# Optimization experiments

Measured on AMD Instinct MI355X. Metric: run time of the kernel, lower is better.

The kernel has to match this reference:

```python
import jax, jax.numpy as jnp
import numpy as np

D, L, DIM, G = 64, 64, 512, 256      # dialogues, utterances/dialogue, feat dim, graph dim
TOPK_FRAC = 0.2
TAU = 0.07


def setup_inputs() -> dict:
    key = jax.random.key(0)
    ks = jax.random.split(key, 7)
    N = D * L
    t = jax.random.normal(ks[0], (N, DIM), dtype=jnp.float32)
    a = jax.random.normal(ks[1], (N, DIM), dtype=jnp.float32)
    v = jax.random.normal(ks[2], (N, DIM), dtype=jnp.float32)
    W_fc = jax.random.normal(ks[3], (DIM, G), dtype=jnp.float32) / np.sqrt(DIM)
    b_fc = jnp.zeros((G,), dtype=jnp.float32)
    W_h = jax.random.normal(ks[4], (G, G), dtype=jnp.float32) / np.sqrt(G)
    b_h = jnp.zeros((G,), dtype=jnp.float32)
    dia_len = np.full((D,), L, dtype=np.int64)  # uniform dialogue lengths
    return {"t": t, "a": a, "v": v, "W_fc": W_fc, "b_fc": b_fc,
            "W_h": W_h, "b_h": b_h, "dia_len": dia_len}


def _contrastive_loss(x, y, tau=TAU):
    # symmetric InfoNCE with matched-index positives
    xn = x / (jnp.linalg.norm(x, axis=-1, keepdims=True) + 1e-8)
    yn = y / (jnp.linalg.norm(y, axis=-1, keepdims=True) + 1e-8)
    sim = (xn @ yn.T) / tau                     # [N, N]
    pos_xy = jnp.diagonal(jax.nn.log_softmax(sim, axis=1))
    pos_yx = jnp.diagonal(jax.nn.log_softmax(sim, axis=0))
    return -(pos_xy.mean() + pos_yx.mean()) / 2.0


def _forward(t, a, v, W_fc, b_fc, W_h, b_h, dia_len):
    dl = np.asarray(dia_len)
    d, l = dl.shape[0], int(dl[0])              # uniform lengths assumed
    m = 3 * l                                   # nodes (and hyperedges) per dialogue
    k = int(l * TOPK_FRAC)
    dim = t.shape[-1]

    # per-dialogue node features in original order [t_i; a_i; v_i]
    feat = jnp.concatenate([t.reshape(d, l, dim),
                            a.reshape(d, l, dim),
                            v.reshape(d, l, dim)], axis=1)   # [d, m, dim]

    # squared euclidean distances (same ordering as torch.cdist for top-k smallest)
    sq = jnp.sum(feat * feat, axis=-1)                        # [d, m]
    d2 = sq[:, :, None] + sq[:, None, :] - 2.0 * jnp.einsum('dmf,dnf->dmn', feat, feat)
    d2 = jax.lax.stop_gradient(jnp.maximum(d2, 0.0))
    _, idx = jax.lax.top_k(-d2, k)                            # [d, m, k] nearest nodes

    # boolean incidence H[d, e, n] = node n participates in hyperedge e
    # (set-union dedup in the original == boolean OR here)
    node_ids = jnp.arange(m)
    H_nb = (idx[..., None] == node_ids).any(axis=2)           # [d, m, m]
    u = node_ids // 3                                         # central utterance of edge j
    cent = ((node_ids[None, :] == u[:, None]) |
            (node_ids[None, :] == u[:, None] + l) |
            (node_ids[None, :] == u[:, None] + 2 * l))        # [m, m]
    H = (H_nb | cent[None]).astype(feat.dtype)                # [d, m, m]

    # fc projection
    X = feat @ W_fc + b_fc                                    # [d, m, G]

    # hypergraph conv: node -> hyperedge (mean) -> node (mean), then Linear+ReLU
    deg_e = H.sum(axis=2, keepdims=True)                      # [d, m, 1]
    E = jnp.einsum('den,dng->deg', H, X) / deg_e              # edge features
    deg_v = H.sum(axis=1)[..., None]                          # [d, m, 1]
    Y = jnp.einsum('den,deg->dng', H, E) / deg_v              # node features
    out = jax.nn.relu(Y @ W_h + b_h)                          # [d, m, G]

    # reverse_features: regroup by modality across dialogues
    tn = out[:, :l].reshape(d * l, -1)
    an = out[:, l:2 * l].reshape(d * l, -1)
    vn = out[:, 2 * l:].reshape(d * l, -1)
    out_cat = jnp.concatenate([tn, an, vn], axis=1)           # [N, 3G]

    loss = (_contrastive_loss(tn, an) + _contrastive_loss(tn, vn)
            + _contrastive_loss(an, vn)) / 3.0
    return out_cat, loss


def reference(t, a, v, W_fc, b_fc, W_h, b_h, dia_len):
    return _forward(t, a, v, W_fc, b_fc, W_h, b_h, dia_len)
```

## Files before the change

### kernel.cpp

```cpp
#include <hip/hip_runtime.h>
#include <math.h>

#define NDIAL 64
#define M3    192
#define DIMF  512
#define GDIM  256
#define NROW  4096
#define TOPK  12
#define INV_TAU (1.0f/0.07f)

typedef __attribute__((ext_vector_type(8))) short bf16x8;
typedef __attribute__((ext_vector_type(4))) float f32x4;
typedef _Float16 f16x8 __attribute__((ext_vector_type(8)));
typedef _Float16 f16x4v __attribute__((ext_vector_type(4)));
typedef __attribute__((address_space(3))) ushort lds_us;
typedef const __attribute__((address_space(1))) ushort gm_us;

__device__ __forceinline__ ushort f2bf(float f) {
    unsigned u = __float_as_uint(f);
    unsigned r = (u + 0x7fff + ((u >> 16) & 1)) >> 16;
    return (ushort)r;
}

template<int KDIM>
__device__ __forceinline__ void mm64bt(
    const float* __restrict__ A, int lda,
    const float* __restrict__ B, int ldb,
    float acc[4][4])
{
    __shared__ float As[64][33];
    __shared__ float Bs[32][68];
    const int tid = threadIdx.x;
    const int tx = tid & 15, ty = tid >> 4;

#pragma unroll
    for (int r = 0; r < 4; r++)
#pragma unroll
        for (int c = 0; c < 4; c++) acc[r][c] = 0.f;

    for (int k0 = 0; k0 < KDIM; k0 += 32) {
#pragma unroll
        for (int i = 0; i < 2; i++) {
            int f = tid + i * 256;
            int m = f >> 3, k4 = f & 7;
            const float4 v4 = *(const float4*)(A + (size_t)m * lda + k0 + k4 * 4);
            As[m][k4 * 4 + 0] = v4.x;
            As[m][k4 * 4 + 1] = v4.y;
            As[m][k4 * 4 + 2] = v4.z;
            As[m][k4 * 4 + 3] = v4.w;
        }
#pragma unroll
        for (int i = 0; i < 2; i++) {
            int f = tid + i * 256;
            int n = f >> 3, k4 = f & 7;
            const float4 v4 = *(const float4*)(B + (size_t)n * ldb + k0 + k4 * 4);
            Bs[k4 * 4 + 0][n] = v4.x;
            Bs[k4 * 4 + 1][n] = v4.y;
            Bs[k4 * 4 + 2][n] = v4.z;
            Bs[k4 * 4 + 3][n] = v4.w;
        }
        __syncthreads();
#pragma unroll
        for (int kk = 0; kk < 32; kk++) {
            float4 b = *(const float4*)&Bs[kk][tx * 4];
#pragma unroll
            for (int r = 0; r < 4; r++) {
                float av = As[ty * 4 + r][kk];
                acc[r][0] += av * b.x;
                acc[r][1] += av * b.y;
                acc[r][2] += av * b.z;
                acc[r][3] += av * b.w;
            }
        }
        __syncthreads();
    }
}

template<int KD, int NW>
__device__ __forceinline__ void hgemm_bt(const _Float16* __restrict__ A, int lda,
                                         const _Float16* __restrict__ B, int ldb,
                                         f32x4 acc[4][4]) {
    __shared__ __align__(16) _Float16 As[64 * 40];
    __shared__ __align__(16) _Float16 Bs[NW * 64 * 40];
    const int tid = threadIdx.x;
    const int lane = tid & 63, w = tid >> 6;
    const int qd = lane >> 4, l15 = lane & 15;

#pragma unroll
    for (int fm = 0; fm < 4; fm++)
#pragma unroll
        for (int fn = 0; fn < 4; fn++)
            acc[fm][fn] = (f32x4){0.f, 0.f, 0.f, 0.f};

    for (int k0 = 0; k0 < KD; k0 += 32) {
        for (int f = tid; f < 256; f += NW * 64) {
            int row = f >> 2, c8 = f & 3;
            *(float4*)&As[row * 40 + c8 * 8] =
                *(const float4*)&A[(size_t)row * lda + k0 + c8 * 8];
        }
#pragma unroll
        for (int i = 0; i < 4; i++) {
            int f = tid + i * NW * 64;
            int row = f >> 2, c8 = f & 3;
            *(float4*)&Bs[row * 40 + c8 * 8] =
                *(const float4*)&B[(size_t)row * ldb + k0 + c8 * 8];
        }
        __syncthreads();
        f16x8 af[4], bfr[4];
#pragma unroll
        for (int fm = 0; fm < 4; fm++)
            af[fm] = *(const f16x8*)&As[(fm * 16 + l15) * 40 + qd * 8];
#pragma unroll
        for (int fn = 0; fn < 4; fn++)
            bfr[fn] = *(const f16x8*)&Bs[(w * 64 + fn * 16 + l15) * 40 + qd * 8];
#pragma unroll
        for (int fm = 0; fm < 4; fm++)
#pragma unroll
            for (int fn = 0; fn < 4; fn++)
                acc[fm][fn] = __builtin_amdgcn_mfma_f32_16x16x32_f16(
                    af[fm], bfr[fn], acc[fm][fn], 0, 0, 0);
        __syncthreads();
    }
}

__device__ __forceinline__ const float* node_ptr(const float* t, const float* a,
                                                 const float* v, int d, int j) {
    int mod = j >> 6, i = j & 63;
    const float* base = (mod == 0) ? t : (mod == 1) ? a : v;
    return base + (size_t)(d * 64 + i) * DIMF;
}

__global__ void kprep(const float* __restrict__ t, const float* __restrict__ a,
                      const float* __restrict__ v, const float* __restrict__ Wfc,
                      const float* __restrict__ Wh, _Float16* __restrict__ featb,
                      _Float16* __restrict__ WfcT, _Float16* __restrict__ WhT,
                      float* __restrict__ sq, float* __restrict__ rs,
                      float* __restrict__ cs, float* __restrict__ degV,
                      _Float16* __restrict__ HbT) {
    int b = blockIdx.x, tid = threadIdx.x;
    if (b < 6144) {
        int e = (b * 256 + tid) * 4;
        int d = e / (M3 * DIMF);
        int rem = e % (M3 * DIMF);
        int n = rem / DIMF, kk = rem % DIMF;
        int mod = n >> 6, i = n & 63;
        const float* src = ((mod == 0) ? t : (mod == 1) ? a : v)
                           + (size_t)(d * 64 + i) * DIMF + kk;
        float4 x = *(const float4*)src;
        f16x4v o = {(_Float16)x.x, (_Float16)x.y, (_Float16)x.z, (_Float16)x.w};
        *(f16x4v*)&featb[e] = o;
    } else if (b < 6272) {
        int e = ((b - 6144) * 256 + tid) * 4;
        int g = e >> 9, kk = e & 511;
        f16x4v o = {(_Float16)Wfc[(size_t)(kk + 0) * GDIM + g],
                    (_Float16)Wfc[(size_t)(kk + 1) * GDIM + g],
                    (_Float16)Wfc[(size_t)(kk + 2) * GDIM + g],
                    (_Float16)Wfc[(size_t)(kk + 3) * GDIM + g]};
        *(f16x4v*)&WfcT[(size_t)g * DIMF + kk] = o;
    } else if (b < 6336) {
        int e = ((b - 6272) * 256 + tid) * 4;
        int go = e >> 8, g = e & 255;
        f16x4v o = {(_Float16)Wh[(size_t)(g + 0) * GDIM + go],
                    (_Float16)Wh[(size_t)(g + 1) * GDIM + go],
                    (_Float16)Wh[(size_t)(g + 2) * GDIM + go],
                    (_Float16)Wh[(size_t)(g + 3) * GDIM + go]};
        *(f16x4v*)&WhT[(size_t)go * GDIM + g] = o;
    } else if (b < 9408) {
        int lane = tid & 63, wv = tid >> 6;
        int n = (b - 6336) * 4 + wv;
        int d = n / M3, j = n % M3;
        const float4* s4 = (const float4*)node_ptr(t, a, v, d, j);
        float s = 0.f;
#pragma unroll
        for (int q = 0; q < 2; q++) {
            float4 x = s4[lane + q * 64];
            s += x.x * x.x + x.y * x.y + x.z * x.z + x.w * x.w;
        }
        for (int o = 32; o; o >>= 1) s += __shfl_down(s, o);
        if (lane == 0) sq[n] = s;
    } else if (b < 9456) {
        int i = (b - 9408) * 256 + tid;
        rs[i] = 0.f; cs[i] = 0.f; degV[i] = 0.f;
    } else {
        int i = (b - 9456) * 256 + tid;
        ulonglong2 z = {0ull, 0ull};
        *(ulonglong2*)&HbT[(size_t)i * 8] = z;
    }
}

__global__ void k1_d2(const float* __restrict__ t, const float* __restrict__ a,
                      const float* __restrict__ v, const float* __restrict__ sq,
                      float* __restrict__ d2) {
    int tileid = blockIdx.x;
    int d = blockIdx.y;
    int bi = (tileid < 3) ? 0 : (tileid < 5) ? 1 : 2;
    int bj = (tileid < 3) ? tileid : (tileid < 5) ? tileid - 2 : 2;
    const float* A = ((bi == 0) ? t : (bi == 1) ? a : v) + (size_t)d * 64 * DIMF;
    const float* B = ((bj == 0) ? t : (bj == 1) ? a : v) + (size_t)d * 64 * DIMF;
    float acc[4][4];
    mm64bt<DIMF>(A, DIMF, B, DIMF, acc);
    int tx = threadIdx.x & 15, ty = threadIdx.x >> 4;
    const float* sqd = sq + d * M3;
    float* outp = d2 + (size_t)d * M3 * M3;
#pragma unroll
    for (int r = 0; r < 4; r++)
#pragma unroll
        for (int c = 0; c < 4; c++) {
            int il = bi * 64 + ty * 4 + r;
            int jl = bj * 64 + tx * 4 + c;
            float vv = fmaxf(sqd[il] + sqd[jl] - 2.f * acc[r][c], 0.f);
            outp[(size_t)il * M3 + jl] = vv;
            if (bi != bj) outp[(size_t)jl * M3 + il] = vv;
        }
}

__global__ void k2_topk(const float* __restrict__ d2, _Float16* __restrict__ Hb,
                        _Float16* __restrict__ HbT, float* __restrict__ degE,
                        float* __restrict__ degV) {
    int lane = threadIdx.x & 63, wv = threadIdx.x >> 6;
    int r = blockIdx.x * 4 + wv;
    int d = r / M3, e = r % M3;
    const float* row = d2 + (size_t)r * M3;
    float w0 = row[lane], w1 = row[lane + 64], w2 = row[lane + 128];
    bool s0 = false, s1 = false, s2 = false;
#pragma unroll
    for (int it = 0; it < TOPK; it++) {
        float bv = w0; int bi = lane;
        if (w1 < bv) { bv = w1; bi = lane + 64; }
        if (w2 < bv) { bv = w2; bi = lane + 128; }
#pragma unroll
        for (int o = 1; o < 64; o <<= 1) {
            float ov = __shfl_xor(bv, o);
            int   oi = __shfl_xor(bi, o);
            if (ov < bv || (ov == bv && oi < bi)) { bv = ov; bi = oi; }
        }
        if (bi == lane)            { s0 = true; w0 = 3.4e38f; }
        else if (bi == lane + 64)  { s1 = true; w1 = 3.4e38f; }
        else if (bi == lane + 128) { s2 = true; w2 = 3.4e38f; }
    }
    int u = e / 3;
    if (lane == u) { s0 = true; s1 = true; s2 = true; }
    float f0 = s0 ? 1.f : 0.f, f1 = s1 ? 1.f : 0.f, f2 = s2 ? 1.f : 0.f;
    _Float16* Hrow = Hb + (size_t)r * M3;
    Hrow[lane] = (_Float16)f0;
    Hrow[lane + 64] = (_Float16)f1;
    Hrow[lane + 128] = (_Float16)f2;
    float cnt = f0 + f1 + f2;
#pragma unroll
    for (int o = 1; o < 64; o <<= 1) cnt += __shfl_xor(cnt, o);
    if (lane == 0) degE[r] = cnt;
    float* dv = degV + d * M3;
    _Float16* HT = HbT + (size_t)d * M3 * M3;
    if (s0) { atomicAdd(&dv[lane], 1.f);       HT[(size_t)lane * M3 + e] = (_Float16)1.f; }
    if (s1) { atomicAdd(&dv[lane + 64], 1.f);  HT[(size_t)(lane + 64) * M3 + e] = (_Float16)1.f; }
    if (s2) { atomicAdd(&dv[lane + 128], 1.f); HT[(size_t)(lane + 128) * M3 + e] = (_Float16)1.f; }
}

__global__ void k3_x(const _Float16* __restrict__ WfcT, const _Float16* __restrict__ featb,
                     const float* __restrict__ bfc, _Float16* __restrict__ XT) {
    int gb = blockIdx.x, d = blockIdx.y;
    const _Float16* A = WfcT + (size_t)gb * 64 * DIMF;
    const _Float16* B = featb + (size_t)d * M3 * DIMF;
    f32x4 acc[4][4];
    hgemm_bt<DIMF, 3>(A, DIMF, B, DIMF, acc);
    int lane = threadIdx.x & 63, w = threadIdx.x >> 6;
    int qd = lane >> 4, l15 = lane & 15;
    _Float16* out = XT + (size_t)d * GDIM * M3;
#pragma unroll
    for (int fm = 0; fm < 4; fm++)
#pragma unroll
        for (int rg = 0; rg < 4; rg++) {
            int g = gb * 64 + fm * 16 + qd * 4 + rg;
            float bias = bfc[g];
#pragma unroll
            for (int fn = 0; fn < 4; fn++) {
                int n = w * 64 + fn * 16 + l15;
                out[(size_t)g * M3 + n] = (_Float16)(acc[fm][fn][rg] + bias);
            }
        }
}

__global__ void k4_E(const _Float16* __restrict__ XT, const _Float16* __restrict__ Hb,
                     const float* __restrict__ degE, _Float16* __restrict__ ET) {
    int gb = blockIdx.x, d = blockIdx.y;
    const _Float16* A = XT + (size_t)d * GDIM * M3 + (size_t)gb * 64 * M3;
    const _Float16* B = Hb + (size_t)d * M3 * M3;
    f32x4 acc[4][4];
    hgemm_bt<M3, 3>(A, M3, B, M3, acc);
    int lane = threadIdx.x & 63, w = threadIdx.x >> 6;
    int qd = lane >> 4, l15 = lane & 15;
    float ide[4];
#pragma unroll
    for (int fn = 0; fn < 4; fn++)
        ide[fn] = 1.f / degE[d * M3 + w * 64 + fn * 16 + l15];
    _Float16* out = ET + (size_t)d * GDIM * M3;
#pragma unroll
    for (int fm = 0; fm < 4; fm++)
#pragma unroll
        for (int rg = 0; rg < 4; rg++) {
            int g = gb * 64 + fm * 16 + qd * 4 + rg;
#pragma unroll
            for (int fn = 0; fn < 4; fn++) {
                int e = w * 64 + fn * 16 + l15;
                out[(size_t)g * M3 + e] = (_Float16)(acc[fm][fn][rg] * ide[fn]);
            }
        }
}

__global__ void k5_Y(const _Float16* __restrict__ HbT, const _Float16* __restrict__ ET,
                     const float* __restrict__ degV, _Float16* __restrict__ Y) {
    int nb = blockIdx.x, d = blockIdx.y;
    const _Float16* A = HbT + (size_t)d * M3 * M3 + (size_t)nb * 64 * M3;
    const _Float16* B = ET + (size_t)d * GDIM * M3;
    f32x4 acc[4][4];
    hgemm_bt<M3, 4>(A, M3, B, M3, acc);
    int lane = threadIdx.x & 63, w = threadIdx.x >> 6;
    int qd = lane >> 4, l15 = lane & 15;
    _Float16* out = Y + ((size_t)d * M3 + nb * 64) * GDIM;
#pragma unroll
    for (int fm = 0; fm < 4; fm++)
#pragma unroll
        for (int rg = 0; rg < 4; rg++) {
            int ml = fm * 16 + qd * 4 + rg;
            float idv = 1.f / degV[d * M3 + nb * 64 + ml];
#pragma unroll
            for (int fn = 0; fn < 4; fn++) {
                int g = w * 64 + fn * 16 + l15;
                out[(size_t)ml * GDIM + g] = (_Float16)(acc[fm][fn][rg] * idv);
            }
        }
}

__global__ void k6_out(const _Float16* __restrict__ Y, const _Float16* __restrict__ WhT,
                       const float* __restrict__ bh, float* __restrict__ outp) {
    int b = blockIdx.x;
    const _Float16* A = Y + (size_t)b * 64 * GDIM;
    f32x4 acc[4][4];
    hgemm_bt<GDIM, 4>(A, GDIM, WhT, GDIM, acc);
    int lane = threadIdx.x & 63, w = threadIdx.x >> 6;
    int qd = lane >> 4, l15 = lane & 15;
    float bb[4];
#pragma unroll
    for (int fn = 0; fn < 4; fn++)
        bb[fn] = bh[w * 64 + fn * 16 + l15];
#pragma unroll
    for (int fm = 0; fm < 4; fm++)
#pragma unroll
        for (int rg = 0; rg < 4; rg++) {
            int r = b * 64 + fm * 16 + qd * 4 + rg;
            int d = r / M3, n = r % M3;
            int mod = n >> 6, i = n & 63;
            float* orow = outp + (size_t)(d * 64 + i) * 768 + mod * GDIM;
#pragma unroll
            for (int fn = 0; fn < 4; fn++) {
                int go = w * 64 + fn * 16 + l15;
                orow[go] = fmaxf(acc[fm][fn][rg] + bb[fn], 0.f);
            }
        }
}

__global__ void k7_norm(const float* __restrict__ outp, ushort* __restrict__ xnb) {
    int lane = threadIdx.x & 63, wv = threadIdx.x >> 6;
    int idx = blockIdx.x * 4 + wv;
    int p = idx / NROW, r = idx % NROW;
    const float4* src = (const float4*)(outp + (size_t)r * 768 + p * GDIM);
    float4 x = src[lane];
    float s = x.x * x.x + x.y * x.y + x.z * x.z + x.w * x.w;
#pragma unroll
    for (int o = 1; o < 64; o <<= 1) s += __shfl_xor(s, o);
    float inv = 1.f / (sqrtf(s) + 1e-8f);
    ushort4 u;
    u.x = f2bf(x.x * inv);
    u.y = f2bf(x.y * inv);
    u.z = f2bf(x.z * inv);
    u.w = f2bf(x.w * inv);
    int c = lane >> 1, h = lane & 1;
    int slot = (c & 24) | ((c & 7) ^ (r & 7));
    *(ushort4*)&xnb[((size_t)p * NROW + r) * GDIM + slot * 8 + h * 4] = u;
}

#define TILE 128
__global__ __launch_bounds__(256) void k9_mfma(const ushort* __restrict__ xnb,
                                               float* __restrict__ rs,
                                               float* __restrict__ cs,
                                               float* __restrict__ diag) {
    int cj = blockIdx.x, ci = blockIdx.y, p = blockIdx.z;
    int px = (p == 2) ? 1 : 0;
    int py = (p == 0) ? 1 : 2;
    const ushort* A = xnb + ((size_t)px * NROW + ci * TILE) * GDIM;
    const ushort* B = xnb + ((size_t)py * NROW + cj * TILE) * GDIM;

    __shared__ __align__(16) ushort As[TILE * 64];
    __shared__ __align__(16) ushort Bs[TILE * 64];

    const int tid = threadIdx.x;
    const int lane = tid & 63, w = tid >> 6;
    const int wrow = w >> 1, wcol = w & 1;
    const int qd = lane >> 4, l15 = lane & 15;
    const int lrow = lane >> 3, lslot = lane & 7;

    f32x4 acc[4][4] = {};

    for (int kh = 0; kh < 4; kh++) {
#pragma unroll
        for (int j = 0; j < 4; j++) {
            int rr = w * 32 + j * 8 + lrow;
            __builtin_amdgcn_global_load_lds(
                (gm_us*)(A + (size_t)rr * GDIM + kh * 64 + lslot * 8),
                (lds_us*)&As[(w * 32 + j * 8) * 64], 16, 0, 0);
            __builtin_amdgcn_global_load_lds(
                (gm_us*)(B + (size_t)rr * GDIM + kh * 64 + lslot * 8),
                (lds_us*)&Bs[(w * 32 + j * 8) * 64], 16, 0, 0);
        }
        __syncthreads();
#pragma unroll
        for (int kk = 0; kk < 2; kk++) {
            bf16x8 af[4], bfv[4];
#pragma unroll
            for (int fm = 0; fm < 4; fm++) {
                int ar = wrow * 64 + fm * 16 + l15;
                af[fm] = *(const bf16x8*)&As[ar * 64 + ((kk * 4 + qd) ^ (ar & 7)) * 8];
            }
#pragma unroll
            for (int fn = 0; fn < 4; fn++) {
                int br = wcol * 64 + fn * 16 + l15;
                bfv[fn] = *(const bf16x8*)&Bs[br * 64 + ((kk * 4 + qd) ^ (br & 7)) * 8];
            }
#pragma unroll
            for (int fm = 0; fm < 4; fm++)
#pragma unroll
                for (int fn = 0; fn < 4; fn++)
                    acc[fm][fn] = __builtin_amdgcn_mfma_f32_16x16x32_bf16(
                        af[fm], bfv[fn], acc[fm][fn], 0, 0, 0);
        }
        __syncthreads();
    }

    float rloc[4][4] = {};
    float cloc[4] = {};
#pragma unroll
    for (int fm = 0; fm < 4; fm++)
#pragma unroll
        for (int fn = 0; fn < 4; fn++)
#pragma unroll
            for (int rg = 0; rg < 4; rg++) {
                float s = acc[fm][fn][rg] * INV_TAU;
                float e = __expf(s);
                rloc[fm][rg] += e;
                cloc[fn] += e;
                if (ci == cj && wrow == wcol && fm == fn && (qd * 4 + rg) == l15)
                    diag[p * NROW + ci * TILE + wrow * 64 + fm * 16 + qd * 4 + rg] = s;
            }
#pragma unroll
    for (int fm = 0; fm < 4; fm++)
#pragma unroll
        for (int rg = 0; rg < 4; rg++) {
            float s = rloc[fm][rg];
            s += __shfl_xor(s, 1);
            s += __shfl_xor(s, 2);
            s += __shfl_xor(s, 4);
            s += __shfl_xor(s, 8);
            if (l15 == 0)
                atomicAdd(&rs[p * NROW + ci * TILE + wrow * 64 + fm * 16 + qd * 4 + rg], s);
        }
#pragma unroll
    for (int fn = 0; fn < 4; fn++) {
        float s = cloc[fn];
        s += __shfl_xor(s, 16);
        s += __shfl_xor(s, 32);
        if (qd == 0)
            atomicAdd(&cs[p * NROW + cj * TILE + wcol * 64 + fn * 16 + l15], s);
    }
}

__global__ void k10_loss(const float* __restrict__ diag, const float* __restrict__ rs,
                         const float* __restrict__ cs, float* __restrict__ outp) {
    float acc = 0.f;
    for (int i = threadIdx.x; i < 3 * NROW; i += 256)
        acc += 2.f * diag[i] - logf(rs[i]) - logf(cs[i]);
    int lane = threadIdx.x & 63, wv = threadIdx.x >> 6;
    for (int o = 32; o; o >>= 1) acc += __shfl_down(acc, o);
    __shared__ float red[4];
    if (lane == 0) red[wv] = acc;
    __syncthreads();
    if (threadIdx.x == 0) {
        float tot = red[0] + red[1] + red[2] + red[3];
        outp[(size_t)NROW * 768] = -tot / (NROW * 6.0f);
    }
}

extern "C" void kernel_launch(void* const* d_in, const int* in_sizes, int n_in,
                              void* d_out, int out_size, void* d_ws, size_t ws_size,
                              hipStream_t stream) {
    const float* t   = (const float*)d_in[0];
    const float* a   = (const float*)d_in[1];
    const float* v   = (const float*)d_in[2];
    const float* Wfc = (const float*)d_in[3];
    const float* bfc = (const float*)d_in[4];
    const float* Wh  = (const float*)d_in[5];
    const float* bh  = (const float*)d_in[6];
    float* outp = (float*)d_out;
    float* ws = (float*)d_ws;

    float* sq    = ws;
    float* d2    = sq + 12288;
    float* HbF   = d2 + 2359296;
    float* HbTF  = HbF + 1179648;
    float* degE  = HbTF + 1179648;
    float* degV  = degE + 12288;
    float* featF = degV + 12288;
    float* WfcTF = featF + 3145728;
    float* WhTF  = WfcTF + 65536;
    float* XTF   = WhTF + 32768;
    float* ETF   = XTF + 1572864;
    float* YF    = ETF + 1572864;
    float* rs    = YF + 1572864;
    float* cs    = rs + 12288;
    float* diag  = cs + 12288;

    _Float16* Hb    = (_Float16*)HbF;
    _Float16* HbT   = (_Float16*)HbTF;
    _Float16* featb = (_Float16*)featF;
    _Float16* WfcT  = (_Float16*)WfcTF;
    _Float16* WhT   = (_Float16*)WhTF;
    _Float16* XT    = (_Float16*)XTF;
    _Float16* ET    = (_Float16*)ETF;
    _Float16* Y     = (_Float16*)YF;
    ushort*   xnb   = (ushort*)d2;

    kprep  <<<10608, 256, 0, stream>>>(t, a, v, Wfc, Wh, featb, WfcT, WhT,
                                       sq, rs, cs, degV, HbT);
    k1_d2  <<<dim3(6, 64), 256, 0, stream>>>(t, a, v, sq, d2);
    k2_topk<<<3072, 256, 0, stream>>>(d2, Hb, HbT, degE, degV);
    k3_x   <<<dim3(4, 64), 192, 0, stream>>>(WfcT, featb, bfc, XT);
    k4_E   <<<dim3(4, 64), 192, 0, stream>>>(XT, Hb, degE, ET);
    k5_Y   <<<dim3(3, 64), 256, 0, stream>>>(HbT, ET, degV, Y);
    k6_out <<<192, 256, 0, stream>>>(Y, WhT, bh, outp);
    k7_norm<<<3072, 256, 0, stream>>>(outp, xnb);
    k9_mfma<<<dim3(32, 32, 3), 256, 0, stream>>>(xnb, rs, cs, diag);
    k10_loss<<<1, 256, 0, stream>>>(diag, rs, cs, outp);
}
```

Measured before the change: 291.7 us.

## Fuse L2 normalization into output GEMM and enlarge similarity GEMM tiles

The row L2 normalization and bf16 swizzled write of the contrastive inputs move into the k6 output kernel, staged through a 64KB shared tile with a per-row sum of squares. This removes the separate k7 launch and its re-read of the fp32 output. The contrastive similarity kernel also grows from 128x128 tiles with 256 threads to 256x256 tiles with 512 threads, which halves redundant operand loads and atomics but uses more registers and LDS and launches fewer blocks. The large shared tile in k6 may limit that kernel's occupancy.

```diff
diff --git a/kernel.cpp b/kernel.cpp
--- a/kernel.cpp
+++ b/kernel.cpp
@@ -11,6 +11,7 @@
 
 typedef __attribute__((ext_vector_type(8))) short bf16x8;
 typedef __attribute__((ext_vector_type(4))) float f32x4;
+typedef __attribute__((ext_vector_type(8))) ushort us8;
 typedef _Float16 f16x8 __attribute__((ext_vector_type(8)));
 typedef _Float16 f16x4v __attribute__((ext_vector_type(4)));
 typedef __attribute__((address_space(3))) ushort lds_us;
@@ -331,14 +332,21 @@
         }
 }
 
-__global__ void k6_out(const _Float16* __restrict__ Y, const _Float16* __restrict__ WhT,
-                       const float* __restrict__ bh, float* __restrict__ outp) {
-    int b = blockIdx.x;
+__global__ __launch_bounds__(256) void k6_out(const _Float16* __restrict__ Y,
+                                              const _Float16* __restrict__ WhT,
+                                              const float* __restrict__ bh,
+                                              float* __restrict__ outp,
+                                              ushort* __restrict__ xnb) {
+    __shared__ float tile[64 * 256];
+    __shared__ float ssq[64];
+    int b = blockIdx.x, tid = threadIdx.x;
+    if (tid < 64) ssq[tid] = 0.f;
     const _Float16* A = Y + (size_t)b * 64 * GDIM;
     f32x4 acc[4][4];
     hgemm_bt<GDIM, 4>(A, GDIM, WhT, GDIM, acc);
-    int lane = threadIdx.x & 63, w = threadIdx.x >> 6;
+    int lane = tid & 63, w = tid >> 6;
     int qd = lane >> 4, l15 = lane & 15;
+    int d = b / 3, mod = b % 3;
     float bb[4];
 #pragma unroll
     for (int fn = 0; fn < 4; fn++)
@@ -347,59 +355,62 @@
     for (int fm = 0; fm < 4; fm++)
 #pragma unroll
         for (int rg = 0; rg < 4; rg++) {
-            int r = b * 64 + fm * 16 + qd * 4 + rg;
-            int d = r / M3, n = r % M3;
-            int mod = n >> 6, i = n & 63;
+            int i = fm * 16 + qd * 4 + rg;
             float* orow = outp + (size_t)(d * 64 + i) * 768 + mod * GDIM;
+            float s2 = 0.f;
 #pragma unroll
             for (int fn = 0; fn < 4; fn++) {
                 int go = w * 64 + fn * 16 + l15;
-                orow[go] = fmaxf(acc[fm][fn][rg] + bb[fn], 0.f);
-            }
-        }
-}
-
-__global__ void k7_norm(const float* __restrict__ outp, ushort* __restrict__ xnb) {
-    int lane = threadIdx.x & 63, wv = threadIdx.x >> 6;
-    int idx = blockIdx.x * 4 + wv;
-    int p = idx / NROW, r = idx % NROW;
-    const float4* src = (const float4*)(outp + (size_t)r * 768 + p * GDIM);
-    float4 x = src[lane];
-    float s = x.x * x.x + x.y * x.y + x.z * x.z + x.w * x.w;
-#pragma unroll
-    for (int o = 1; o < 64; o <<= 1) s += __shfl_xor(s, o);
-    float inv = 1.f / (sqrtf(s) + 1e-8f);
-    ushort4 u;
-    u.x = f2bf(x.x * inv);
-    u.y = f2bf(x.y * inv);
-    u.z = f2bf(x.z * inv);
-    u.w = f2bf(x.w * inv);
-    int c = lane >> 1, h = lane & 1;
-    int slot = (c & 24) | ((c & 7) ^ (r & 7));
-    *(ushort4*)&xnb[((size_t)p * NROW + r) * GDIM + slot * 8 + h * 4] = u;
-}
-
-#define TILE 128
-__global__ __launch_bounds__(256) void k9_mfma(const ushort* __restrict__ xnb,
-                                               float* __restrict__ rs,
-                                               float* __restrict__ cs,
-                                               float* __restrict__ diag) {
+                float vv = fmaxf(acc[fm][fn][rg] + bb[fn], 0.f);
+                orow[go] = vv;
+                tile[i * 256 + go] = vv;
+                s2 += vv * vv;
+            }
+            s2 += __shfl_xor(s2, 1);
+            s2 += __shfl_xor(s2, 2);
+            s2 += __shfl_xor(s2, 4);
+            s2 += __shfl_xor(s2, 8);
+            if (l15 == 0) atomicAdd(&ssq[i], s2);
+        }
+    __syncthreads();
+    if (tid < 64) ssq[tid] = 1.f / (sqrtf(ssq[tid]) + 1e-8f);
+    __syncthreads();
+#pragma unroll
+    for (int it = 0; it < 8; it++) {
+        int f = tid + it * 256;
+        int row = f >> 5, c = f & 31;
+        float4 xa = *(const float4*)&tile[row * 256 + c * 8];
+        float4 xb = *(const float4*)&tile[row * 256 + c * 8 + 4];
+        float iv = ssq[row];
+        us8 o = {f2bf(xa.x * iv), f2bf(xa.y * iv), f2bf(xa.z * iv), f2bf(xa.w * iv),
+                 f2bf(xb.x * iv), f2bf(xb.y * iv), f2bf(xb.z * iv), f2bf(xb.w * iv)};
+        int rx = d * 64 + row;
+        int slot = (c & 24) | ((c & 7) ^ (row & 7));
+        *(us8*)&xnb[((size_t)mod * NROW + rx) * GDIM + slot * 8] = o;
+    }
+}
+
+#define TILE2 256
+__global__ __launch_bounds__(512, 2) void k9_mfma(const ushort* __restrict__ xnb,
+                                                  float* __restrict__ rs,
+                                                  float* __restrict__ cs,
+                                                  float* __restrict__ diag) {
     int cj = blockIdx.x, ci = blockIdx.y, p = blockIdx.z;
     int px = (p == 2) ? 1 : 0;
     int py = (p == 0) ? 1 : 2;
-    const ushort* A = xnb + ((size_t)px * NROW + ci * TILE) * GDIM;
-    const ushort* B = xnb + ((size_t)py * NROW + cj * TILE) * GDIM;
-
-    __shared__ __align__(16) ushort As[TILE * 64];
-    __shared__ __align__(16) ushort Bs[TILE * 64];
+    const ushort* A = xnb + ((size_t)px * NROW + ci * TILE2) * GDIM;
+    const ushort* B = xnb + ((size_t)py * NROW + cj * TILE2) * GDIM;
+
+    __shared__ __align__(16) ushort As[TILE2 * 64];
+    __shared__ __align__(16) ushort Bs[TILE2 * 64];
 
     const int tid = threadIdx.x;
     const int lane = tid & 63, w = tid >> 6;
-    const int wrow = w >> 1, wcol = w & 1;
+    const int wrow = w >> 2, wcol = w & 3;
     const int qd = lane >> 4, l15 = lane & 15;
     const int lrow = lane >> 3, lslot = lane & 7;
 
-    f32x4 acc[4][4] = {};
+    f32x4 acc[8][4] = {};
 
     for (int kh = 0; kh < 4; kh++) {
 #pragma unroll
@@ -415,10 +426,10 @@
         __syncthreads();
 #pragma unroll
         for (int kk = 0; kk < 2; kk++) {
-            bf16x8 af[4], bfv[4];
-#pragma unroll
-            for (int fm = 0; fm < 4; fm++) {
-                int ar = wrow * 64 + fm * 16 + l15;
+            bf16x8 af[8], bfv[4];
+#pragma unroll
+            for (int fm = 0; fm < 8; fm++) {
+                int ar = wrow * 128 + fm * 16 + l15;
                 af[fm] = *(const bf16x8*)&As[ar * 64 + ((kk * 4 + qd) ^ (ar & 7)) * 8];
             }
 #pragma unroll
@@ -427,7 +438,7 @@
                 bfv[fn] = *(const bf16x8*)&Bs[br * 64 + ((kk * 4 + qd) ^ (br & 7)) * 8];
             }
 #pragma unroll
-            for (int fm = 0; fm < 4; fm++)
+            for (int fm = 0; fm < 8; fm++)
 #pragma unroll
                 for (int fn = 0; fn < 4; fn++)
                     acc[fm][fn] = __builtin_amdgcn_mfma_f32_16x16x32_bf16(
@@ -436,10 +447,10 @@
         __syncthreads();
     }
 
-    float rloc[4][4] = {};
+    float rloc[8][4] = {};
     float cloc[4] = {};
 #pragma unroll
-    for (int fm = 0; fm < 4; fm++)
+    for (int fm = 0; fm < 8; fm++)
 #pragma unroll
         for (int fn = 0; fn < 4; fn++)
 #pragma unroll
@@ -448,11 +459,12 @@
                 float e = __expf(s);
                 rloc[fm][rg] += e;
                 cloc[fn] += e;
-                if (ci == cj && wrow == wcol && fm == fn && (qd * 4 + rg) == l15)
-                    diag[p * NROW + ci * TILE + wrow * 64 + fm * 16 + qd * 4 + rg] = s;
-            }
-#pragma unroll
-    for (int fm = 0; fm < 4; fm++)
+                int grow = ci * TILE2 + wrow * 128 + fm * 16 + qd * 4 + rg;
+                int gcol = cj * TILE2 + wcol * 64 + fn * 16 + l15;
+                if (grow == gcol) diag[p * NROW + grow] = s;
+            }
+#pragma unroll
+    for (int fm = 0; fm < 8; fm++)
 #pragma unroll
         for (int rg = 0; rg < 4; rg++) {
             float s = rloc[fm][rg];
@@ -461,7 +473,7 @@
             s += __shfl_xor(s, 4);
             s += __shfl_xor(s, 8);
             if (l15 == 0)
-                atomicAdd(&rs[p * NROW + ci * TILE + wrow * 64 + fm * 16 + qd * 4 + rg], s);
+                atomicAdd(&rs[p * NROW + ci * TILE2 + wrow * 128 + fm * 16 + qd * 4 + rg], s);
         }
 #pragma unroll
     for (int fn = 0; fn < 4; fn++) {
@@ -469,7 +481,7 @@
         s += __shfl_xor(s, 16);
         s += __shfl_xor(s, 32);
         if (qd == 0)
-            atomicAdd(&cs[p * NROW + cj * TILE + wcol * 64 + fn * 16 + l15], s);
+            atomicAdd(&cs[p * NROW + cj * TILE2 + wcol * 64 + fn * 16 + l15], s);
     }
 }
 
@@ -535,8 +547,7 @@
     k3_x   <<<dim3(4, 64), 192, 0, stream>>>(WfcT, featb, bfc, XT);
     k4_E   <<<dim3(4, 64), 192, 0, stream>>>(XT, Hb, degE, ET);
     k5_Y   <<<dim3(3, 64), 256, 0, stream>>>(HbT, ET, degV, Y);
-    k6_out <<<192, 256, 0, stream>>>(Y, WhT, bh, outp);
-    k7_norm<<<3072, 256, 0, stream>>>(outp, xnb);
-    k9_mfma<<<dim3(32, 32, 3), 256, 0, stream>>>(xnb, rs, cs, diag);
+    k6_out <<<192, 256, 0, stream>>>(Y, WhT, bh, outp, xnb);
+    k9_mfma<<<dim3(16, 16, 3), 512, 0, stream>>>(xnb, rs, cs, diag);
     k10_loss<<<1, 256, 0, stream>>>(diag, rs, cs, outp);
 }
```

New measurement: 288.9 us. About the same (-0.9%).
